# Kernel optimization log

Measured on AMD Instinct MI355X. Metric: run time of the kernel, lower is better.

Reference implementation:

```python
import jax, jax.numpy as jnp
import numpy as np
from math import sqrt

D_MODEL = 1024
N_HEADS = 16
FFN = 4096
B, N = 2, 2048
EPS = 1e-5


def _layernorm(x, g, b):
    mu = jnp.mean(x, -1, keepdims=True)
    var = jnp.mean((x - mu) ** 2, -1, keepdims=True)
    return (x - mu) * jax.lax.rsqrt(var + EPS) * g + b


def setup_inputs() -> dict:
    key = jax.random.key(0)
    ks = jax.random.split(key, 12)
    s = 1.0 / sqrt(D_MODEL)
    sf = 1.0 / sqrt(FFN)
    inp = {
        "tgt": jax.random.normal(ks[0], (B, N, D_MODEL), jnp.float32),
        # True = masked. Causal: query i may attend to keys j <= i.
        "tgt_mask": jnp.triu(jnp.ones((N, N), jnp.bool_), k=1),
        "tgt_key_pad_mask": jnp.zeros((B, N), jnp.bool_),
        "Wq": jax.random.uniform(ks[1], (D_MODEL, D_MODEL), jnp.float32, -s, s),
        "Wk": jax.random.uniform(ks[2], (D_MODEL, D_MODEL), jnp.float32, -s, s),
        "Wv": jax.random.uniform(ks[3], (D_MODEL, D_MODEL), jnp.float32, -s, s),
        "Wo": jax.random.uniform(ks[4], (D_MODEL, D_MODEL), jnp.float32, -s, s),
        "bo": jax.random.uniform(ks[5], (D_MODEL,), jnp.float32, -s, s),
        "W1": jax.random.uniform(ks[6], (FFN, D_MODEL), jnp.float32, -s, s),
        "b1": jax.random.uniform(ks[7], (FFN,), jnp.float32, -s, s),
        "W2": jax.random.uniform(ks[8], (D_MODEL, FFN), jnp.float32, -sf, sf),
        "b2": jax.random.uniform(ks[9], (D_MODEL,), jnp.float32, -sf, sf),
        "g1": jnp.ones((D_MODEL,), jnp.float32),
        "beta1": jnp.zeros((D_MODEL,), jnp.float32),
        "g2": jnp.ones((D_MODEL,), jnp.float32),
        "beta2": jnp.zeros((D_MODEL,), jnp.float32),
    }
    return inp


def _mha(x, tgt_mask, pad_mask, Wq, Wk, Wv, Wo, bo):
    b, n, d = x.shape
    dk = d // N_HEADS
    q = (x @ Wq.T).reshape(b, n, N_HEADS, dk).transpose(0, 2, 1, 3)  # bhnd
    k = (x @ Wk.T).reshape(b, n, N_HEADS, dk).transpose(0, 2, 1, 3)
    v = (x @ Wv.T).reshape(b, n, N_HEADS, dk).transpose(0, 2, 1, 3)
    scores = jnp.einsum("bhqd,bhkd->bhqk", q, k) / sqrt(dk)
    mask = tgt_mask[None, None, :, :] | pad_mask[:, None, None, :]
    scores = jnp.where(mask, -jnp.inf, scores)
    att = jax.nn.softmax(scores, axis=-1)
    out = jnp.einsum("bhqk,bhkd->bhqd", att, v).transpose(0, 2, 1, 3).reshape(b, n, d)
    return out @ Wo.T + bo


def reference(tgt, tgt_mask, tgt_key_pad_mask, Wq, Wk, Wv, Wo, bo,
              W1, b1, W2, b2, g1, beta1, g2, beta2):
    # PostNorm logic (pre_norm=False), dropout=0 (eval)
    h = _mha(tgt, tgt_mask, tgt_key_pad_mask, Wq, Wk, Wv, Wo, bo)
    x = _layernorm(tgt + h, g1, beta1)
    m = jax.nn.gelu(x @ W1.T + b1, approximate=True) @ W2.T + b2
    return _layernorm(x + m, g2, beta2)
```

## Files before the change

### kernel.cpp

```cpp
#include <hip/hip_runtime.h>


#define DEV __device__ __forceinline__

typedef __attribute__((ext_vector_type(4)))  float f32x4;
typedef __attribute__((ext_vector_type(16))) float f32x16;
typedef __attribute__((ext_vector_type(8)))  short s16x8;

static constexpr int Bb   = 2;
static constexpr int NN   = 2048;
static constexpr int DM   = 1024;
static constexpr int HH   = 16;
static constexpr int DK   = 64;
static constexpr int FF   = 4096;
static constexpr int ROWS = Bb * NN;

#define AS1(p) ((const __attribute__((address_space(1))) void*)(p))
#define AS3(p) ((__attribute__((address_space(3))) void*)(p))

DEV unsigned short f2bf(float f) {
  unsigned u = __float_as_uint(f);
  u += 0x7fff + ((u >> 16) & 1);
  return (unsigned short)(u >> 16);
}
DEV float fexp2(float x) {
  float r;
  asm("v_exp_f32 %0, %1" : "=v"(r) : "v"(x));
  return r;
}
DEV unsigned cvtpk(float lo, float hi) {
  unsigned r;
  asm("v_cvt_pk_bf16_f32 %0, %1, %2" : "=v"(r) : "v"(lo), "v"(hi));
  return r;
}

__global__ __launch_bounds__(256) void k_cast(const float* __restrict__ in,
                                              ushort* __restrict__ out, int n4) {
  int i = blockIdx.x * 256 + threadIdx.x;
  if (i >= n4) return;
  float4 v = reinterpret_cast<const float4*>(in)[i];
  ushort4 o;
  o.x = f2bf(v.x); o.y = f2bf(v.y); o.z = f2bf(v.z); o.w = f2bf(v.w);
  reinterpret_cast<ushort4*>(out)[i] = o;
}

template <int EPI, int BN, bool QKV>
__global__ __launch_bounds__(256) void k_gemm(
    const ushort* __restrict__ A, const ushort* __restrict__ Bt,
    const float* __restrict__ bias, const float* __restrict__ resid,
    ushort* __restrict__ Cb, float* __restrict__ Cf,
    int K, int nbx) {
  __shared__ ushort As[2][128][32];
  __shared__ ushort Bs[2][BN][32];

  const int t = threadIdx.x;
  const int lane = t & 63, w = t >> 6;
  const int lr = lane & 15, lg = lane >> 4;
  const int lrow = lane >> 2, lc8 = (lane & 3) * 8;

  const int nwg = gridDim.x;
  const int bid = blockIdx.x;
  const int q8 = nwg >> 3, r8 = nwg & 7;
  const int xcd = bid & 7, lin = bid >> 3;
  const int wg = (xcd < r8 ? xcd * (q8 + 1) : r8 * (q8 + 1) + (xcd - r8) * q8) + lin;
  const int band = wg / (4 * nbx);
  const int inn  = wg % (4 * nbx);
  const int by = band * 4 + (inn & 3);
  const int bx = inn >> 2;

  const int bRow = by * 128;
  const int bCol = bx * BN;

  constexpr int NW = BN / 32;
  const int wRow = (w >> 1) * 64, wCol = (w & 1) * (BN / 2);

  const f32x4 zero = {0.f, 0.f, 0.f, 0.f};
  f32x4 acc[4][NW];
#pragma unroll
  for (int m = 0; m < 4; ++m)
#pragma unroll
    for (int n = 0; n < NW; ++n) acc[m][n] = zero;

  auto stage = [&](int buf, int kt) {
#pragma unroll
    for (int i = 0; i < 2; ++i) {
      int rr = w * 32 + i * 16;
      __builtin_amdgcn_global_load_lds(
          AS1(A + (size_t)(bRow + rr + lrow) * K + kt + lc8),
          AS3(&As[buf][rr][0]), 16, 0, 0);
    }
#pragma unroll
    for (int i = 0; i < BN / 64; ++i) {
      int rr = w * (BN / 4) + i * 16;
      __builtin_amdgcn_global_load_lds(
          AS1(Bt + (size_t)(bCol + rr + lrow) * K + kt + lc8),
          AS3(&Bs[buf][rr][0]), 16, 0, 0);
    }
  };

  stage(0, 0);
  const int nk = K / 32;
  for (int tt = 0; tt < nk; ++tt) {
    const int cur = tt & 1;
    __syncthreads();
    if (tt + 1 < nk) stage(cur ^ 1, (tt + 1) * 32);

    s16x8 af[4], bfr[NW];
#pragma unroll
    for (int m = 0; m < 4; ++m)
      af[m] = *reinterpret_cast<const s16x8*>(&As[cur][wRow + m * 16 + lr][lg * 8]);
#pragma unroll
    for (int n = 0; n < NW; ++n)
      bfr[n] = *reinterpret_cast<const s16x8*>(&Bs[cur][wCol + n * 16 + lr][lg * 8]);
#pragma unroll
    for (int m = 0; m < 4; ++m)
#pragma unroll
      for (int n = 0; n < NW; ++n)
        acc[m][n] = __builtin_amdgcn_mfma_f32_16x16x32_bf16(af[m], bfr[n], acc[m][n], 0, 0, 0);
  }

  ushort* CbOut = Cb;
  int colBase = bCol, Ncols = nbx * BN, third = 0;
  if (QKV) {
    third = bCol >> 10;
    CbOut = Cb + (size_t)third * ROWS * DM;
    colBase = bCol & 1023;
    Ncols = DM;
  }
#pragma unroll
  for (int m = 0; m < 4; ++m) {
    int gr = bRow + wRow + m * 16 + lg * 4;
#pragma unroll
    for (int n = 0; n < NW; ++n) {
      int gc = colBase + wCol + n * 16 + lr;
      float bv = (EPI == 1 || EPI == 2) ? bias[gc] : 0.0f;
#pragma unroll
      for (int r = 0; r < 4; ++r) {
        int nr = gr + r;
        float v = acc[m][n][r] + bv;
        if (EPI == 2) {
          size_t idx = (size_t)nr * Ncols + gc;
          Cf[idx] = v + resid[idx];
        } else if (EPI == 1) {
          size_t idx = (size_t)nr * Ncols + gc;
          float u = v + 0.044715f * v * v * v;
          float g = v / (1.0f + __expf(-1.5957691216057308f * u));
          CbOut[idx] = f2bf(g);
        } else {
          int gcs = gc;
          if (QKV && third == 1)
            gcs = (gc & ~63) | ((gc ^ ((nr & 7) << 3)) & 63);
          CbOut[(size_t)nr * Ncols + gcs] = f2bf(v);
        }
      }
    }
  }
}

__global__ __launch_bounds__(256) void k_vt(const ushort* __restrict__ V,
                                            ushort* __restrict__ vT) {
  __shared__ ushort Ls[64][72];
  const int t = threadIdx.x;
  const int n0 = blockIdx.x * 64;
  const int bh = blockIdx.y;
  const int b = bh >> 4, h = bh & 15;
  const int n = t >> 2;
#pragma unroll
  for (int half = 0; half < 2; ++half) {
    int c8 = ((t & 3) + half * 4) * 8;
    int4 v = *reinterpret_cast<const int4*>(
        V + ((size_t)(b * NN + n0 + n)) * DM + h * DK + c8);
    *reinterpret_cast<int4*>(&Ls[n][c8]) = v;
  }
  __syncthreads();
  const int d = t >> 2;
#pragma unroll
  for (int half = 0; half < 2; ++half) {
    int c = (t & 3) + half * 4;
    ushort tmp[8];
#pragma unroll
    for (int j = 0; j < 8; ++j) tmp[j] = Ls[c * 8 + j][d];
    size_t out = ((size_t)bh * DK + d) * NN + n0 + ((c ^ (d & 7)) * 8);
    *reinterpret_cast<int4*>(vT + out) = *reinterpret_cast<const int4*>(tmp);
  }
}

template <int WB>
__global__ __launch_bounds__(256) void k_ln(const float* __restrict__ in,
                                            const float* __restrict__ g,
                                            const float* __restrict__ bta,
                                            float* __restrict__ outf,
                                            ushort* __restrict__ outb) {
  const int row = blockIdx.x;
  const int t = threadIdx.x;
  float4 v = reinterpret_cast<const float4*>(in + (size_t)row * DM)[t];
  float s1 = v.x + v.y + v.z + v.w;
  float s2 = v.x * v.x + v.y * v.y + v.z * v.z + v.w * v.w;
#pragma unroll
  for (int m = 32; m; m >>= 1) {
    s1 += __shfl_xor(s1, m, 64);
    s2 += __shfl_xor(s2, m, 64);
  }
  __shared__ float red[2][4];
  if ((t & 63) == 0) { red[0][t >> 6] = s1; red[1][t >> 6] = s2; }
  __syncthreads();
  s1 = red[0][0] + red[0][1] + red[0][2] + red[0][3];
  s2 = red[1][0] + red[1][1] + red[1][2] + red[1][3];
  const float mu = s1 * (1.0f / DM);
  const float var = s2 * (1.0f / DM) - mu * mu;
  const float rstd = rsqrtf(var + 1e-5f);
  float4 gv = reinterpret_cast<const float4*>(g)[t];
  float4 bv = reinterpret_cast<const float4*>(bta)[t];
  float4 o;
  o.x = (v.x - mu) * rstd * gv.x + bv.x;
  o.y = (v.y - mu) * rstd * gv.y + bv.y;
  o.z = (v.z - mu) * rstd * gv.z + bv.z;
  o.w = (v.w - mu) * rstd * gv.w + bv.w;
  reinterpret_cast<float4*>(outf + (size_t)row * DM)[t] = o;
  if (WB) {
    ushort4 ob;
    ob.x = f2bf(o.x); ob.y = f2bf(o.y); ob.z = f2bf(o.z); ob.w = f2bf(o.w);
    reinterpret_cast<ushort4*>(outb + (size_t)row * DM)[t] = ob;
  }
}

__global__ __launch_bounds__(256) void k_attn(const ushort* __restrict__ Q,
                                              const ushort* __restrict__ Kb,
                                              const ushort* __restrict__ vT,
                                              ushort* __restrict__ O) {
  __shared__ ushort Ks[2][64 * 64];
  __shared__ ushort Vs[2][64 * 64];

  const int t = threadIdx.x;
  const int qi = (NN / 128 - 1) - (int)blockIdx.x;
  const int bh = blockIdx.y;
  const int lane = t & 63, wid = t >> 6;
  const int l31 = lane & 31, hi = lane >> 5;
  const int q0w = qi * 128 + wid * 32;
  const size_t base = (size_t)bh * NN * DM / HH * HH;
  const size_t qbase = ((size_t)(bh >> 4) * NN) * DM + (bh & 15) * DK;
  const size_t vbase = (size_t)bh * DK * NN;
  (void)base;

  const float C = 0.18033688011112043f;

  s16x8 qf[4];
#pragma unroll
  for (int c = 0; c < 4; ++c)
    qf[c] = *reinterpret_cast<const s16x8*>(Q + qbase + (size_t)(q0w + l31) * DM + c * 16 + hi * 8);

  float mrun = -1e30f, lrun = 0.f, negcm = 1e30f;
  f32x16 accO[2];
#pragma unroll
  for (int dt = 0; dt < 2; ++dt)
#pragma unroll
    for (int r = 0; r < 16; ++r) accO[dt][r] = 0.f;

  auto stage = [&](int buf, int kt) {
    const int kk = kt * 64;
#pragma unroll
    for (int i = 0; i < 2; ++i) {
      int row0 = wid * 16 + i * 8;
      __builtin_amdgcn_global_load_lds(
          AS1(Kb + qbase + (size_t)(kk + row0 + (lane >> 3)) * DM + (lane & 7) * 8),
          AS3(&Ks[buf][row0 * 64]), 16, 0, 0);
      __builtin_amdgcn_global_load_lds(
          AS1(vT + vbase + (size_t)(row0 + (lane >> 3)) * NN + kk + (lane & 7) * 8),
          AS3(&Vs[buf][row0 * 64]), 16, 0, 0);
    }
  };

  const int nkt = 2 * qi + 2;
  stage(0, 0);
  for (int kt = 0; kt < nkt; ++kt) {
    const int cur = kt & 1;
    const int kk = kt * 64;
    __syncthreads();
    if (kt + 1 < nkt) stage(cur ^ 1, kt + 1);

    if (kk <= q0w + 31) {
      const char* KsB = (const char*)Ks[cur];
      const char* VsB = (const char*)Vs[cur];
      const bool diag = (kk + 64 > q0w);
      const int nsub = (kk + 32 <= q0w + 31) ? 2 : 1;

      f32x16 st[2];
#pragma unroll
      for (int sub = 0; sub < 2; ++sub) {
        if (sub >= nsub) break;
#pragma unroll
        for (int r = 0; r < 16; ++r) st[sub][r] = 0.f;
        const int row = sub * 32 + l31;
        const int swz = (row & 7) << 4;
#pragma unroll
        for (int c = 0; c < 4; ++c) {
          s16x8 kf = *reinterpret_cast<const s16x8*>(KsB + row * 128 + ((c * 32 + hi * 16) ^ swz));
          st[sub] = __builtin_amdgcn_mfma_f32_32x32x16_bf16(kf, qf[c], st[sub], 0, 0, 0);
        }
      }

      const int q = q0w + l31;
      float p[32];
#pragma unroll
      for (int sub = 0; sub < 2; ++sub) {
        if (sub >= nsub) break;
#pragma unroll
        for (int r = 0; r < 16; ++r) {
          float v = st[sub][r];
          if (diag) {
            int kl = sub * 32 + (r & 3) + 8 * (r >> 2) + 4 * hi;
            if (kk + kl > q) v = -1e30f;
          }
          p[sub * 16 + r] = v;
        }
      }
      float a[16];
#pragma unroll
      for (int i = 0; i < 16; ++i) a[i] = (nsub == 2) ? fmaxf(p[i], p[i + 16]) : p[i];
#pragma unroll
      for (int s = 8; s; s >>= 1)
#pragma unroll
        for (int i = 0; i < 8; ++i) if (i < s) a[i] = fmaxf(a[i], a[i + s]);
      float rm = fmaxf(a[0], __shfl_xor(a[0], 32, 64));

      if (__any(rm > mrun)) {
        const float mn = fmaxf(mrun, rm);
        const float alpha = fexp2(C * (mrun - mn));
        mrun = mn;
        negcm = -C * mn;
        lrun *= alpha;
#pragma unroll
        for (int dt = 0; dt < 2; ++dt) accO[dt] *= alpha;
      }

#pragma unroll
      for (int sub = 0; sub < 2; ++sub) {
        if (sub >= nsub) break;
#pragma unroll
        for (int i = 0; i < 16; ++i)
          p[sub * 16 + i] = fexp2(fmaf(p[sub * 16 + i], C, negcm));
      }
#pragma unroll
      for (int i = 0; i < 16; ++i) a[i] = (nsub == 2) ? (p[i] + p[i + 16]) : p[i];
#pragma unroll
      for (int s = 8; s; s >>= 1)
#pragma unroll
        for (int i = 0; i < 8; ++i) if (i < s) a[i] += a[i + s];
      lrun += a[0] + __shfl_xor(a[0], 32, 64);

      s16x8 pf[4];
#pragma unroll
      for (int sub = 0; sub < 2; ++sub) {
        if (sub >= nsub) break;
#pragma unroll
        for (int half = 0; half < 2; ++half) {
          const float* pp = &p[sub * 16 + half * 8];
          unsigned X0 = cvtpk(pp[0], pp[1]);
          unsigned X1 = cvtpk(pp[2], pp[3]);
          unsigned Y0 = cvtpk(pp[4], pp[5]);
          unsigned Y1 = cvtpk(pp[6], pp[7]);
          asm volatile("v_permlane32_swap_b32 %0, %1" : "+v"(X0), "+v"(Y0));
          asm volatile("v_permlane32_swap_b32 %0, %1" : "+v"(X1), "+v"(Y1));
          union { unsigned u[4]; s16x8 v; } uu;
          uu.u[0] = X0; uu.u[1] = X1; uu.u[2] = Y0; uu.u[3] = Y1;
          pf[sub * 2 + half] = uu.v;
        }
      }

#pragma unroll
      for (int dt = 0; dt < 2; ++dt) {
        const int d = dt * 32 + l31;
        const int vswz = (d & 7) << 4;
#pragma unroll
        for (int kc = 0; kc < 4; ++kc) {
          if (kc >= nsub * 2) break;
          s16x8 vf = *reinterpret_cast<const s16x8*>(VsB + d * 128 + ((kc * 32 + hi * 16) ^ vswz));
          accO[dt] = __builtin_amdgcn_mfma_f32_32x32x16_bf16(vf, pf[kc], accO[dt], 0, 0, 0);
        }
      }
    }
  }

  const int q = q0w + l31;
  const float inv = 1.0f / lrun;
#pragma unroll
  for (int dt = 0; dt < 2; ++dt)
#pragma unroll
    for (int rg = 0; rg < 4; ++rg) {
      int d0 = 8 * rg + 4 * hi + 32 * dt;
      ushort4 ov;
      ov.x = f2bf(accO[dt][rg * 4 + 0] * inv);
      ov.y = f2bf(accO[dt][rg * 4 + 1] * inv);
      ov.z = f2bf(accO[dt][rg * 4 + 2] * inv);
      ov.w = f2bf(accO[dt][rg * 4 + 3] * inv);
      *reinterpret_cast<ushort4*>(O + qbase + (size_t)q * DM + d0) = ov;
    }
}

extern "C" void kernel_launch(void* const* d_in, const int* in_sizes, int n_in,
                              void* d_out, int out_size, void* d_ws, size_t ws_size,
                              hipStream_t stream) {
  const float* tgt = (const float*)d_in[0];
  const float* Wq  = (const float*)d_in[3];
  const float* Wk  = (const float*)d_in[4];
  const float* Wv  = (const float*)d_in[5];
  const float* Wo  = (const float*)d_in[6];
  const float* bo  = (const float*)d_in[7];
  const float* W1  = (const float*)d_in[8];
  const float* b1  = (const float*)d_in[9];
  const float* W2  = (const float*)d_in[10];
  const float* b2  = (const float*)d_in[11];
  const float* g1  = (const float*)d_in[12];
  const float* be1 = (const float*)d_in[13];
  const float* g2  = (const float*)d_in[14];
  const float* be2 = (const float*)d_in[15];

  char* ws = (char*)d_ws;
  size_t off = 0;
  auto alloc = [&](size_t bytes) {
    void* p = ws + off;
    off += (bytes + 255) & ~(size_t)255;
    return p;
  };
  ushort* xb   = (ushort*)alloc((size_t)ROWS * DM * 2);
  ushort* wqb  = (ushort*)alloc((size_t)DM * DM * 2);
  ushort* wkb  = (ushort*)alloc((size_t)DM * DM * 2);
  ushort* wvb  = (ushort*)alloc((size_t)DM * DM * 2);
  ushort* wob  = (ushort*)alloc((size_t)DM * DM * 2);
  ushort* w1b  = (ushort*)alloc((size_t)FF * DM * 2);
  ushort* w2b  = (ushort*)alloc((size_t)DM * FF * 2);
  ushort* qbuf = (ushort*)alloc((size_t)ROWS * DM * 2);
  ushort* kbuf = (ushort*)alloc((size_t)ROWS * DM * 2);
  ushort* vbuf = (ushort*)alloc((size_t)ROWS * DM * 2);
  ushort* vtb  = (ushort*)alloc((size_t)ROWS * DM * 2);
  ushort* atnb = (ushort*)alloc((size_t)ROWS * DM * 2);
  float*  h1   = (float*)alloc((size_t)ROWS * DM * 4);
  float*  x1f  = (float*)alloc((size_t)ROWS * DM * 4);
  ushort* x1b  = (ushort*)alloc((size_t)ROWS * DM * 2);
  ushort* t1b  = (ushort*)alloc((size_t)ROWS * FF * 2);
  (void)ws_size; (void)in_sizes; (void)n_in; (void)out_size;
  (void)wkb; (void)wvb; (void)kbuf;

  auto cast = [&](const float* src, ushort* dst, size_t n) {
    int n4 = (int)(n / 4);
    k_cast<<<dim3((n4 + 255) / 256), 256, 0, stream>>>(src, dst, n4);
  };
  cast(tgt, xb, (size_t)ROWS * DM);
  cast(Wq, wqb, (size_t)DM * DM);
  cast(Wk, wkb, (size_t)DM * DM);
  cast(Wv, wvb, (size_t)DM * DM);
  cast(Wo, wob, (size_t)DM * DM);
  cast(W1, w1b, (size_t)FF * DM);
  cast(W2, w2b, (size_t)DM * FF);

  dim3 blk(256);
  k_gemm<0, 128, true><<<dim3(24 * 32), blk, 0, stream>>>(
      xb, wqb, nullptr, nullptr, qbuf, nullptr, DM, 24);

  k_vt<<<dim3(NN / 64, Bb * HH), blk, 0, stream>>>(vbuf, vtb);

  k_attn<<<dim3(NN / 128, Bb * HH), blk, 0, stream>>>(qbuf, kbuf, vtb, atnb);

  k_gemm<2, 64, false><<<dim3(16 * 32), blk, 0, stream>>>(
      atnb, wob, bo, tgt, nullptr, h1, DM, 16);
  k_ln<1><<<dim3(ROWS), blk, 0, stream>>>(h1, g1, be1, x1f, x1b);

  k_gemm<1, 128, false><<<dim3(32 * 32), blk, 0, stream>>>(
      x1b, w1b, b1, nullptr, t1b, nullptr, DM, 32);
  float* z = h1;
  k_gemm<2, 64, false><<<dim3(16 * 32), blk, 0, stream>>>(
      t1b, w2b, b2, x1f, nullptr, z, FF, 16);
  k_ln<0><<<dim3(ROWS), blk, 0, stream>>>(z, g2, be2, (float*)d_out, nullptr);
}
```

Baseline: 305.3 us.

## Split attention KV loop across two wave groups and merge softmax states

The attention block grows to 512 threads, with two groups of four waves each handling alternating 64-key tiles (even and odd) for the same 128 queries, each using its own double-buffered LDS. At the end, group 1 writes its partial output accumulators and running max/sum to LDS, and group 0 rescales and merges them before storing. This halves the sequential KV loop length per wave and raises parallelism for the causal attention kernel. The cost is extra LDS, a reduction step through shared memory, and possible imbalance, since the diagonal tiles fall unevenly across the two groups.

```diff
diff --git a/kernel.cpp b/kernel.cpp
--- a/kernel.cpp
+++ b/kernel.cpp
@@ -224,23 +224,24 @@
   }
 }
 
-__global__ __launch_bounds__(256) void k_attn(const ushort* __restrict__ Q,
-                                              const ushort* __restrict__ Kb,
-                                              const ushort* __restrict__ vT,
-                                              ushort* __restrict__ O) {
-  __shared__ ushort Ks[2][64 * 64];
-  __shared__ ushort Vs[2][64 * 64];
+__global__ __launch_bounds__(512, 4) void k_attn(const ushort* __restrict__ Q,
+                                                 const ushort* __restrict__ Kb,
+                                                 const ushort* __restrict__ vT,
+                                                 ushort* __restrict__ O) {
+  __shared__ ushort Ks[2][2][64 * 64];
+  __shared__ ushort Vs[2][2][64 * 64];
 
   const int t = threadIdx.x;
   const int qi = (NN / 128 - 1) - (int)blockIdx.x;
   const int bh = blockIdx.y;
-  const int lane = t & 63, wid = t >> 6;
+  const int lane = t & 63;
+  const int wid8 = t >> 6;
+  const int half = wid8 >> 2;
+  const int wid = wid8 & 3;
   const int l31 = lane & 31, hi = lane >> 5;
   const int q0w = qi * 128 + wid * 32;
-  const size_t base = (size_t)bh * NN * DM / HH * HH;
   const size_t qbase = ((size_t)(bh >> 4) * NN) * DM + (bh & 15) * DK;
   const size_t vbase = (size_t)bh * DK * NN;
-  (void)base;
 
   const float C = 0.18033688011112043f;
 
@@ -263,24 +264,24 @@
       int row0 = wid * 16 + i * 8;
       __builtin_amdgcn_global_load_lds(
           AS1(Kb + qbase + (size_t)(kk + row0 + (lane >> 3)) * DM + (lane & 7) * 8),
-          AS3(&Ks[buf][row0 * 64]), 16, 0, 0);
+          AS3(&Ks[half][buf][row0 * 64]), 16, 0, 0);
       __builtin_amdgcn_global_load_lds(
           AS1(vT + vbase + (size_t)(row0 + (lane >> 3)) * NN + kk + (lane & 7) * 8),
-          AS3(&Vs[buf][row0 * 64]), 16, 0, 0);
+          AS3(&Vs[half][buf][row0 * 64]), 16, 0, 0);
     }
   };
 
-  const int nkt = 2 * qi + 2;
-  stage(0, 0);
-  for (int kt = 0; kt < nkt; ++kt) {
-    const int cur = kt & 1;
-    const int kk = kt * 64;
+  const int nj = qi + 1;
+  stage(0, half);
+  for (int j = 0; j < nj; ++j) {
+    const int cur = j & 1;
+    const int kk = (2 * j + half) * 64;
     __syncthreads();
-    if (kt + 1 < nkt) stage(cur ^ 1, kt + 1);
+    if (j + 1 < nj) stage(cur ^ 1, 2 * (j + 1) + half);
 
     if (kk <= q0w + 31) {
-      const char* KsB = (const char*)Ks[cur];
-      const char* VsB = (const char*)Vs[cur];
+      const char* KsB = (const char*)&Ks[half][cur][0];
+      const char* VsB = (const char*)&Vs[half][cur][0];
       const bool diag = (kk + 64 > q0w);
       const int nsub = (kk + 32 <= q0w + 31) ? 2 : 1;
 
@@ -353,8 +354,8 @@
       for (int sub = 0; sub < 2; ++sub) {
         if (sub >= nsub) break;
 #pragma unroll
-        for (int half = 0; half < 2; ++half) {
-          const float* pp = &p[sub * 16 + half * 8];
+        for (int hf = 0; hf < 2; ++hf) {
+          const float* pp = &p[sub * 16 + hf * 8];
           unsigned X0 = cvtpk(pp[0], pp[1]);
           unsigned X1 = cvtpk(pp[2], pp[3]);
           unsigned Y0 = cvtpk(pp[4], pp[5]);
@@ -363,7 +364,7 @@
           asm volatile("v_permlane32_swap_b32 %0, %1" : "+v"(X1), "+v"(Y1));
           union { unsigned u[4]; s16x8 v; } uu;
           uu.u[0] = X0; uu.u[1] = X1; uu.u[2] = Y0; uu.u[3] = Y1;
-          pf[sub * 2 + half] = uu.v;
+          pf[sub * 2 + hf] = uu.v;
         }
       }
 
@@ -381,20 +382,49 @@
     }
   }
 
-  const int q = q0w + l31;
-  const float inv = 1.0f / lrun;
-#pragma unroll
-  for (int dt = 0; dt < 2; ++dt)
-#pragma unroll
-    for (int rg = 0; rg < 4; ++rg) {
-      int d0 = 8 * rg + 4 * hi + 32 * dt;
-      ushort4 ov;
-      ov.x = f2bf(accO[dt][rg * 4 + 0] * inv);
-      ov.y = f2bf(accO[dt][rg * 4 + 1] * inv);
-      ov.z = f2bf(accO[dt][rg * 4 + 2] * inv);
-      ov.w = f2bf(accO[dt][rg * 4 + 3] * inv);
-      *reinterpret_cast<ushort4*>(O + qbase + (size_t)q * DM + d0) = ov;
-    }
+  __syncthreads();
+  float* mO  = (float*)&Ks[0][0][0];
+  float* mlS = (float*)&Vs[0][0][0];
+  const int lbase = (wid * 64 + lane) * 32;
+  const int swz = (lane & 7) << 4;
+  char* lreg = (char*)mO + (size_t)lbase * 4;
+
+  if (half == 1) {
+#pragma unroll
+    for (int dt = 0; dt < 2; ++dt)
+#pragma unroll
+      for (int i = 0; i < 4; ++i) {
+        f32x4 v4 = { accO[dt][i * 4 + 0], accO[dt][i * 4 + 1],
+                     accO[dt][i * 4 + 2], accO[dt][i * 4 + 3] };
+        *reinterpret_cast<f32x4*>(lreg + ((dt * 64 + i * 16) ^ swz)) = v4;
+      }
+    mlS[(wid * 64 + lane) * 2 + 0] = mrun;
+    mlS[(wid * 64 + lane) * 2 + 1] = lrun;
+  }
+  __syncthreads();
+
+  if (half == 0) {
+    const float m1 = mlS[(wid * 64 + lane) * 2 + 0];
+    const float l1 = mlS[(wid * 64 + lane) * 2 + 1];
+    const float mN = fmaxf(mrun, m1);
+    const float s0 = fexp2(C * (mrun - mN));
+    const float s1 = fexp2(C * (m1 - mN));
+    const float inv = 1.0f / (lrun * s0 + l1 * s1);
+    const int q = q0w + l31;
+#pragma unroll
+    for (int dt = 0; dt < 2; ++dt)
+#pragma unroll
+      for (int rg = 0; rg < 4; ++rg) {
+        f32x4 o1 = *reinterpret_cast<const f32x4*>(lreg + ((dt * 64 + rg * 16) ^ swz));
+        int d0 = 8 * rg + 4 * hi + 32 * dt;
+        ushort4 ov;
+        ov.x = f2bf((accO[dt][rg * 4 + 0] * s0 + o1[0] * s1) * inv);
+        ov.y = f2bf((accO[dt][rg * 4 + 1] * s0 + o1[1] * s1) * inv);
+        ov.z = f2bf((accO[dt][rg * 4 + 2] * s0 + o1[2] * s1) * inv);
+        ov.w = f2bf((accO[dt][rg * 4 + 3] * s0 + o1[3] * s1) * inv);
+        *reinterpret_cast<ushort4*>(O + qbase + (size_t)q * DM + d0) = ov;
+      }
+  }
 }
 
 extern "C" void kernel_launch(void* const* d_in, const int* in_sizes, int n_in,
@@ -459,7 +489,7 @@
 
   k_vt<<<dim3(NN / 64, Bb * HH), blk, 0, stream>>>(vbuf, vtb);
 
-  k_attn<<<dim3(NN / 128, Bb * HH), blk, 0, stream>>>(qbuf, kbuf, vtb, atnb);
+  k_attn<<<dim3(NN / 128, Bb * HH), dim3(512), 0, stream>>>(qbuf, kbuf, vtb, atnb);
 
   k_gemm<2, 64, false><<<dim3(16 * 32), blk, 0, stream>>>(
       atnb, wob, bo, tgt, nullptr, h1, DM, 16);
```

Result: slower. 315.7 us (+3.4%).
